# Performance work log

Hardware: AMD Instinct MI355X
Metric: run time of the kernel (lower is better)

Reference implementation:

```python
import jax, jax.numpy as jnp
import numpy as np

BN_EPS = 1e-5

def _bn(x, gamma, beta):
    # BatchNorm1d in training mode: batch mean / biased variance over nodes
    m = x.mean(axis=0)
    v = x.var(axis=0)
    return gamma * (x - m) * jax.lax.rsqrt(v + BN_EPS) + beta

def setup_inputs() -> dict:
    key = jax.random.key(0)
    ks = jax.random.split(key, 16)
    N, E, G = 50000, 600000, 1000
    A, H, O, L = 64, 128, 256, 3
    x = jax.random.normal(ks[0], (N, A), dtype=jnp.float32)
    edge_index = jax.random.randint(ks[1], (2, E), 0, N, dtype=jnp.int64)
    batch_index = jnp.sort(jax.random.randint(ks[2], (N,), 0, G, dtype=jnp.int64))
    s = 1.0 / np.sqrt(H)
    params = {
        "emb_W": jax.random.normal(ks[3], (A, H), jnp.float32) / np.sqrt(A),
        "emb_b": jnp.zeros((H,), jnp.float32),
        "W1": jax.random.normal(ks[4], (L, H, H), jnp.float32) * s,
        "b1": jnp.zeros((L, H), jnp.float32),
        "g1": jnp.ones((L, H), jnp.float32),
        "be1": jnp.zeros((L, H), jnp.float32),
        "W2": jax.random.normal(ks[5], (L, H, H), jnp.float32) * s,
        "b2": jnp.zeros((L, H), jnp.float32),
        "g2": jnp.ones((L, H), jnp.float32),
        "be2": jnp.zeros((L, H), jnp.float32),
        "eps": jnp.zeros((L,), jnp.float32),
        "proj_W": jax.random.normal(ks[6], (H, O), jnp.float32) * s,
        "proj_b": jnp.zeros((O,), jnp.float32),
    }
    return dict(x=x, edge_index=edge_index, batch_index=batch_index, num_graphs=G, **params)

def reference(x, edge_index, batch_index, num_graphs, emb_W, emb_b,
              W1, b1, g1, be1, W2, b2, g2, be2, eps, proj_W, proj_b):
    N = x.shape[0]
    row, col = edge_index[0], edge_index[1]
    h = x @ emb_W + emb_b  # [N, H]
    L = W1.shape[0]
    for l in range(L):
        # gather neighbor feats + scatter-add aggregation
        agg = jax.ops.segment_sum(h[col], row, num_segments=N)
        z = (1.0 + eps[l]) * h + agg
        z = jax.nn.relu(_bn(z @ W1[l] + b1[l], g1[l], be1[l]))
        h = jax.nn.relu(_bn(z @ W2[l] + b2[l], g2[l], be2[l]))
    # graph readout: scatter-add nodes into per-graph sums
    pooled = jax.ops.segment_sum(h, batch_index, num_segments=num_graphs)  # [G, H]
    return pooled @ proj_W + proj_b  # [G, O]
```

## Files before the change

### kernel.cpp

```cpp
#include <hip/hip_runtime.h>
#include <stdint.h>

#define NN 50000
#define NE 600000
#define NG 1000
#define AD 64
#define HD 128
#define OD 256
#define BN_EPS_F 1e-5f
#define INV_N (1.0f / 50000.0f)
#define NB 196
#define FILLB 586
#define PREWB 416
#define NCOPY 32
#define SREG (NCOPY * 256)

typedef __attribute__((ext_vector_type(8))) short  mbf16x8;
typedef __attribute__((ext_vector_type(4))) float  mf32x4;
typedef __attribute__((ext_vector_type(4))) unsigned short mu16x4;
typedef __attribute__((ext_vector_type(4))) unsigned int   mu32x4;

__device__ __forceinline__ float bf2f(unsigned short u) {
    union { unsigned int i; float f; } v; v.i = ((unsigned int)u) << 16; return v.f;
}
__device__ __forceinline__ unsigned short f2bf(float f) {
    union { float f; unsigned int i; } v; v.f = f;
    unsigned int r = v.i + 0x7fffu + ((v.i >> 16) & 1u);
    return (unsigned short)(r >> 16);
}
__device__ __forceinline__ void bn_ss(
    const float* stats, const float* __restrict__ gamma,
    const float* __restrict__ beta, int c, float& sc, float& sh)
{
    const float mean = stats[c] * INV_N;
    const float var = fmaxf(stats[128 + c] * INV_N - mean * mean, 0.f);
    const float inv = rsqrtf(var + BN_EPS_F);
    sc = gamma[c] * inv;
    sh = beta[c] - mean * sc;
}
__device__ __forceinline__ float fold_stat(const float* __restrict__ reg, int t)
{
    float a = 0.f;
#pragma unroll
    for (int c = 0; c < NCOPY; c++) a += reg[c * 256 + t];
    return a;
}

__global__ __launch_bounds__(256) void prew_kernel(
    const float* __restrict__ emb_W, const float* __restrict__ W1,
    const float* __restrict__ W2, unsigned short* __restrict__ wt,
    float* __restrict__ stats, const int* __restrict__ ei,
    int* __restrict__ deg)
{
    if ((int)blockIdx.x >= PREWB) {
        const int e0 = ((blockIdx.x - PREWB) * 256 + threadIdx.x) * 4;
        if (e0 < NE) {
            const int4 rv = *(const int4*)(ei + e0);
            if ((unsigned)rv.x < NN) atomicAdd(&deg[rv.x], 1);
            if ((unsigned)rv.y < NN) atomicAdd(&deg[rv.y], 1);
            if ((unsigned)rv.z < NN) atomicAdd(&deg[rv.z], 1);
            if ((unsigned)rv.w < NN) atomicAdd(&deg[rv.w], 1);
        }
        return;
    }
    const int t = blockIdx.x * 256 + threadIdx.x;
    if (t < 6 * SREG) stats[t] = 0.f;
    if (t < 8192) {
        wt[t] = f2bf(emb_W[(t & 63) * 128 + (t >> 6)]);
    } else {
        const int t2 = t - 8192;
        if (t2 >= 6 * 16384) return;
        const int which = t2 >> 14, o = t2 & 16383;
        const int n = o >> 7, k = o & 127;
        const float* src = (which < 3) ? (W1 + (size_t)which * 16384)
                                       : (W2 + (size_t)(which - 3) * 16384);
        wt[t] = f2bf(src[k * 128 + n]);
    }
}

template <int K, int RG, int AMODE, bool SOUT, int TAIL>
__global__ __launch_bounds__(256) void gemm_kernel(
    const void* __restrict__ in, const unsigned short* __restrict__ Wt,
    const float* __restrict__ bias, const float* __restrict__ stats_in,
    const float* __restrict__ gamma, const float* __restrict__ beta,
    unsigned short* __restrict__ out, float* __restrict__ stats_out, int n_rows,
    const int* __restrict__ t_a, int* __restrict__ t_b, int* __restrict__ t_c)
{
    constexpr int TAILB = (TAIL == 1) ? FILLB : (TAIL == 2) ? NB : 0;
    if (TAIL != 0 && (int)blockIdx.x < TAILB) {
        const int t = blockIdx.x * 256 + threadIdx.x;
        if constexpr (TAIL == 1) {
            const int e0 = t * 4;
            if (e0 < NE) {
                const int4 rv = *(const int4*)(t_a + e0);
                const int4 cv = *(const int4*)(t_a + NE + e0);
                if ((unsigned)rv.x < NN && (unsigned)cv.x < NN)
                    t_c[atomicAdd(&t_b[rv.x], 1)] = cv.x;
                if ((unsigned)rv.y < NN && (unsigned)cv.y < NN)
                    t_c[atomicAdd(&t_b[rv.y], 1)] = cv.y;
                if ((unsigned)rv.z < NN && (unsigned)cv.z < NN)
                    t_c[atomicAdd(&t_b[rv.z], 1)] = cv.z;
                if ((unsigned)rv.w < NN && (unsigned)cv.w < NN)
                    t_c[atomicAdd(&t_b[rv.w], 1)] = cv.w;
            }
        } else {
            if (t < NN) {
                int b = t_a[t];
                int pb = (t == 0) ? -1 : t_a[t - 1];
                if (b > NG - 1) b = NG - 1;
                if (pb > NG - 1) pb = NG - 1;
                for (int g = pb + 1; g <= b; g++) t_b[g] = t;
                if (t == NN - 1)
                    for (int g = b + 1; g <= NG; g++) t_b[g] = NN;
            }
        }
        return;
    }
    const int bid = blockIdx.x - TAILB;

    constexpr int ROWS = RG * 64;
    constexpr int SA = K + 8;
    __shared__ unsigned short zs[ROWS * SA];
    __shared__ float ssl[128], ssh[128];
    __shared__ float lsum[128], lsq[128];
    __shared__ float sarr[256];

    const int tid = threadIdx.x;
    const int wave = tid >> 6, lane = tid & 63;
    const int row0 = bid * ROWS;

    if (SOUT && tid < 128) { lsum[tid] = 0.f; lsq[tid] = 0.f; }
    if (AMODE == 2) {
        sarr[tid] = fold_stat(stats_in, tid);
        __syncthreads();
        if (tid < 128) {
            float sc, sh; bn_ss(sarr, gamma, beta, tid, sc, sh);
            ssl[tid] = sc; ssh[tid] = sh;
        }
        __syncthreads();
    }

    if constexpr (AMODE == 0) {
        const float* src = (const float*)in;
        constexpr int LPR = K / 4;
        for (int i = tid; i < ROWS * LPR; i += 256) {
            const int r = i / LPR, c4 = (i % LPR) * 4;
            mf32x4 v = {0.f, 0.f, 0.f, 0.f};
            if (row0 + r < n_rows)
                v = *(const mf32x4*)(src + (size_t)(row0 + r) * K + c4);
            mu16x4 o;
            o[0] = f2bf(v[0]); o[1] = f2bf(v[1]); o[2] = f2bf(v[2]); o[3] = f2bf(v[3]);
            *(mu16x4*)(&zs[r * SA + c4]) = o;
        }
    } else {
        const unsigned short* src = (const unsigned short*)in;
        constexpr int LPR = K / 8;
        float sc[8], sh[8];
        if constexpr (AMODE == 2) {
            const int c8 = (tid % LPR) * 8;
#pragma unroll
            for (int j = 0; j < 8; j++) { sc[j] = ssl[c8 + j]; sh[j] = ssh[c8 + j]; }
        }
        for (int i = tid; i < ROWS * LPR; i += 256) {
            const int r = i / LPR, c8 = (i % LPR) * 8;
            mu32x4 v = {0, 0, 0, 0};
            if (row0 + r < n_rows)
                v = *(const mu32x4*)(src + (size_t)(row0 + r) * K + c8);
            if constexpr (AMODE == 2) {
                const unsigned short* u = (const unsigned short*)&v;
                mu16x4 oa, ob;
#pragma unroll
                for (int j = 0; j < 4; j++)
                    oa[j] = f2bf(fmaxf(bf2f(u[j]) * sc[j] + sh[j], 0.f));
#pragma unroll
                for (int j = 0; j < 4; j++)
                    ob[j] = f2bf(fmaxf(bf2f(u[4 + j]) * sc[4 + j] + sh[4 + j], 0.f));
                *(mu16x4*)(&zs[r * SA + c8]) = oa;
                *(mu16x4*)(&zs[r * SA + c8 + 4]) = ob;
            } else {
                *(mu32x4*)(&zs[r * SA + c8]) = v;
            }
        }
    }
    __syncthreads();

    mf32x4 acc[RG][8];
#pragma unroll
    for (int g = 0; g < RG; g++)
#pragma unroll
        for (int t = 0; t < 8; t++) acc[g][t] = {0.f, 0.f, 0.f, 0.f};
    const int kq = (lane >> 4) * 8;
    int mrow[RG];
#pragma unroll
    for (int g = 0; g < RG; g++) mrow[g] = wave * (16 * RG) + g * 16 + (lane & 15);
    const unsigned short* wn = Wt + (lane & 15) * K;
#pragma unroll 1
    for (int kk = 0; kk < K / 32; kk++) {
        const int k0 = kk * 32 + kq;
        mbf16x8 a[RG];
#pragma unroll
        for (int g = 0; g < RG; g++) a[g] = *(const mbf16x8*)(&zs[mrow[g] * SA + k0]);
        mbf16x8 bfr[8];
#pragma unroll
        for (int t = 0; t < 8; t++) bfr[t] = *(const mbf16x8*)(wn + t * 16 * K + k0);
#pragma unroll
        for (int t = 0; t < 8; t++)
#pragma unroll
            for (int g = 0; g < RG; g++)
                acc[g][t] = __builtin_amdgcn_mfma_f32_16x16x32_bf16(
                    a[g], bfr[t], acc[g][t], 0, 0, 0);
    }

#pragma unroll
    for (int g = 0; g < RG; g++) {
        const int rbase = wave * (16 * RG) + g * 16 + ((lane >> 4) << 2);
#pragma unroll
        for (int t = 0; t < 8; t++) {
            const int c = t * 16 + (lane & 15);
            const float bv = bias[c];
            float s = 0.f, q = 0.f;
#pragma unroll
            for (int r = 0; r < 4; r++) {
                const int grow = row0 + rbase + r;
                const float y = acc[g][t][r] + bv;
                if (grow < n_rows) {
                    out[(size_t)grow * 128 + c] = f2bf(y);
                    if (SOUT) { s += y; q += y * y; }
                }
            }
            if (SOUT) {
                s += __shfl_xor(s, 16); s += __shfl_xor(s, 32);
                q += __shfl_xor(q, 16); q += __shfl_xor(q, 32);
                if ((lane >> 4) == 0) {
                    atomicAdd(&lsum[c], s);
                    atomicAdd(&lsq[c], q);
                }
            }
        }
    }
    if (SOUT) {
        __syncthreads();
        float* cb = stats_out + (bid & (NCOPY - 1)) * 256;
        if (tid < 128) {
            atomicAdd(&cb[tid], lsum[tid]);
            atomicAdd(&cb[128 + tid], lsq[tid]);
        }
    }
}

__global__ __launch_bounds__(256) void bscan_kernel(
    const int* __restrict__ deg, int* __restrict__ rowptr, int* __restrict__ bsum)
{
    __shared__ int sm[256];
    const int t = threadIdx.x, idx = blockIdx.x * 256 + t;
    const int d = (idx < NN) ? deg[idx] : 0;
    sm[t] = d; __syncthreads();
    for (int ofs = 1; ofs < 256; ofs <<= 1) {
        int v = (t >= ofs) ? sm[t - ofs] : 0;
        __syncthreads();
        sm[t] += v;
        __syncthreads();
    }
    if (idx < NN) rowptr[idx] = sm[t] - d;
    if (t == 255) bsum[blockIdx.x] = sm[255];
}

__global__ __launch_bounds__(256) void scanfix_kernel(
    const int* __restrict__ bsum, int* __restrict__ rowptr, int* __restrict__ cursor)
{
    __shared__ int sm[256];
    const int t = threadIdx.x;
    const int d = (t < NB) ? bsum[t] : 0;
    sm[t] = d; __syncthreads();
    for (int ofs = 1; ofs < 256; ofs <<= 1) {
        int v = (t >= ofs) ? sm[t - ofs] : 0;
        __syncthreads();
        sm[t] += v;
        __syncthreads();
    }
    const int boff = (blockIdx.x == 0) ? 0 : sm[blockIdx.x - 1];
    const int idx = blockIdx.x * 256 + t;
    if (idx < NN) {
        const int v = rowptr[idx] + boff;
        rowptr[idx] = v;
        cursor[idx] = v;
    }
    if (blockIdx.x == NB - 1 && t == 0) rowptr[NN] = sm[NB - 1];
}

template <bool BN>
__global__ __launch_bounds__(256) void gather_kernel(
    const unsigned short* __restrict__ src, const int* __restrict__ rowptr,
    const int* __restrict__ adj, const float* __restrict__ stats,
    const float* __restrict__ gamma, const float* __restrict__ beta,
    const float* __restrict__ eps, int l, unsigned short* __restrict__ z)
{
    __shared__ float sarr[256];
    if constexpr (BN) {
        sarr[threadIdx.x] = fold_stat(stats, threadIdx.x);
        __syncthreads();
    }
    const int node = blockIdx.x * 16 + (threadIdx.x >> 4);
    const int c0 = (threadIdx.x & 15) * 8;
    if (node >= NN) return;
    float sc[8], sh[8];
    if (BN) {
#pragma unroll
        for (int j = 0; j < 8; j++) bn_ss(sarr, gamma, beta, c0 + j, sc[j], sh[j]);
    }
    const float e = 1.0f + eps[l];
    float acc[8];
    {
        mu32x4 v = *(const mu32x4*)(src + (size_t)node * HD + c0);
        const unsigned short* u = (const unsigned short*)&v;
#pragma unroll
        for (int j = 0; j < 8; j++) {
            float f = bf2f(u[j]);
            if (BN) f = fmaxf(f * sc[j] + sh[j], 0.f);
            acc[j] = e * f;
        }
    }
    const int s = rowptr[node], t = rowptr[node + 1];
    int i = s;
    for (; i + 4 <= t; i += 4) {
        const int n0 = adj[i], n1 = adj[i + 1], n2 = adj[i + 2], n3 = adj[i + 3];
        mu32x4 v0 = *(const mu32x4*)(src + (size_t)n0 * HD + c0);
        mu32x4 v1 = *(const mu32x4*)(src + (size_t)n1 * HD + c0);
        mu32x4 v2 = *(const mu32x4*)(src + (size_t)n2 * HD + c0);
        mu32x4 v3 = *(const mu32x4*)(src + (size_t)n3 * HD + c0);
        const unsigned short* u0 = (const unsigned short*)&v0;
        const unsigned short* u1 = (const unsigned short*)&v1;
        const unsigned short* u2 = (const unsigned short*)&v2;
        const unsigned short* u3 = (const unsigned short*)&v3;
#pragma unroll
        for (int j = 0; j < 8; j++) {
            float f0 = bf2f(u0[j]), f1 = bf2f(u1[j]);
            float f2 = bf2f(u2[j]), f3 = bf2f(u3[j]);
            if (BN) {
                f0 = fmaxf(f0 * sc[j] + sh[j], 0.f);
                f1 = fmaxf(f1 * sc[j] + sh[j], 0.f);
                f2 = fmaxf(f2 * sc[j] + sh[j], 0.f);
                f3 = fmaxf(f3 * sc[j] + sh[j], 0.f);
            }
            acc[j] += (f0 + f1) + (f2 + f3);
        }
    }
    for (; i < t; i++) {
        mu32x4 v = *(const mu32x4*)(src + (size_t)adj[i] * HD + c0);
        const unsigned short* u = (const unsigned short*)&v;
#pragma unroll
        for (int j = 0; j < 8; j++) {
            float f = bf2f(u[j]);
            if (BN) f = fmaxf(f * sc[j] + sh[j], 0.f);
            acc[j] += f;
        }
    }
    mu16x4 o0, o1;
#pragma unroll
    for (int j = 0; j < 4; j++) o0[j] = f2bf(acc[j]);
#pragma unroll
    for (int j = 0; j < 4; j++) o1[j] = f2bf(acc[4 + j]);
    *(mu16x4*)(z + (size_t)node * HD + c0) = o0;
    *(mu16x4*)(z + (size_t)node * HD + c0 + 4) = o1;
}

__global__ __launch_bounds__(256) void poolfinal_kernel(
    const unsigned short* __restrict__ y, const int* __restrict__ start,
    const float* __restrict__ stats, const float* __restrict__ gamma,
    const float* __restrict__ beta, const float* __restrict__ pw,
    const float* __restrict__ pb, float* __restrict__ out)
{
    __shared__ float red[16][128];
    __shared__ float pl[128];
    __shared__ float sarr[256];
    sarr[threadIdx.x] = fold_stat(stats, threadIdx.x);
    __syncthreads();
    const int g = blockIdx.x;
    const int rg = threadIdx.x >> 4;
    const int c0 = (threadIdx.x & 15) * 8;
    float sc[8], sh[8];
#pragma unroll
    for (int j = 0; j < 8; j++) bn_ss(sarr, gamma, beta, c0 + j, sc[j], sh[j]);
    int s = start[g], e = start[g + 1];
    if (s < 0) s = 0;
    if (e > NN) e = NN;
    float acc[8];
#pragma unroll
    for (int j = 0; j < 8; j++) acc[j] = 0.f;
    for (int n = s + rg; n < e; n += 16) {
        mu32x4 v = *(const mu32x4*)(y + (size_t)n * HD + c0);
        const unsigned short* u = (const unsigned short*)&v;
#pragma unroll
        for (int j = 0; j < 8; j++)
            acc[j] += fmaxf(bf2f(u[j]) * sc[j] + sh[j], 0.f);
    }
#pragma unroll
    for (int j = 0; j < 8; j++) red[rg][c0 + j] = acc[j];
    __syncthreads();
    if (threadIdx.x < 128) {
        float a = 0.f;
#pragma unroll
        for (int k = 0; k < 16; k++) a += red[k][threadIdx.x];
        pl[threadIdx.x] = a;
    }
    __syncthreads();
    const int o = threadIdx.x;
    float facc = pb[o];
#pragma unroll 4
    for (int k = 0; k < 128; k++) facc += pl[k] * pw[k * 256 + o];
    out[(size_t)g * 256 + o] = facc;
}

extern "C" void kernel_launch(void* const* d_in, const int* in_sizes, int n_in,
                              void* d_out, int out_size, void* d_ws, size_t ws_size,
                              hipStream_t stream)
{
    const float* x      = (const float*)d_in[0];
    const int*   edge   = (const int*)d_in[1];
    const int*   batch  = (const int*)d_in[2];
    const float* emb_W  = (const float*)d_in[4];
    const float* emb_b  = (const float*)d_in[5];
    const float* W1     = (const float*)d_in[6];
    const float* b1     = (const float*)d_in[7];
    const float* g1     = (const float*)d_in[8];
    const float* be1    = (const float*)d_in[9];
    const float* W2     = (const float*)d_in[10];
    const float* b2     = (const float*)d_in[11];
    const float* g2     = (const float*)d_in[12];
    const float* be2    = (const float*)d_in[13];
    const float* eps    = (const float*)d_in[14];
    const float* proj_W = (const float*)d_in[15];
    const float* proj_b = (const float*)d_in[16];
    float* out = (float*)d_out;

    char* ws = (char*)d_ws;
    size_t off = 0;
    auto take = [&](size_t bytes) -> char* {
        char* p = ws + off;
        off += (bytes + 255) & ~(size_t)255;
        return p;
    };
    float*          stats  = (float*)take(6 * SREG * 4);
    int*            start  = (int*)take((NG + 1) * 4);
    int*            deg    = (int*)take(NN * 4);
    int*            rowptr = (int*)take((NN + 1) * 4);
    int*            cursor = (int*)take(NN * 4);
    int*            bsum   = (int*)take(256 * 4);
    unsigned short* wt     = (unsigned short*)take((size_t)(8192 + 6 * 16384) * 2);
    int*            adj    = (int*)take((size_t)NE * 4);
    unsigned short* zbuf   = (unsigned short*)take((size_t)NN * HD * 2);
    unsigned short* y1buf  = (unsigned short*)take((size_t)NN * HD * 2);
    unsigned short* y2buf  = (unsigned short*)take((size_t)NN * HD * 2);

    const int eg_grid = (NN + 63) / 64;
    const int lg_grid = (NN + 127) / 128;
    auto st = [&](int r) { return stats + (size_t)r * SREG; };

    hipMemsetAsync(deg, 0, NN * 4, stream);
    prew_kernel<<<PREWB + FILLB, 256, 0, stream>>>(
        emb_W, W1, W2, wt, stats, edge, deg);
    bscan_kernel<<<NB, 256, 0, stream>>>(deg, rowptr, bsum);
    scanfix_kernel<<<NB, 256, 0, stream>>>(bsum, rowptr, cursor);

    gemm_kernel<AD, 1, 0, false, 1><<<FILLB + eg_grid, 256, 0, stream>>>(
        x, wt, emb_b, nullptr, nullptr, nullptr, y2buf, nullptr, NN,
        edge, cursor, adj);

    for (int l = 0; l < 3; l++) {
        if (l == 0)
            gather_kernel<false><<<(NN + 15) / 16, 256, 0, stream>>>(
                y2buf, rowptr, adj, nullptr, nullptr, nullptr, eps, l, zbuf);
        else
            gather_kernel<true><<<(NN + 15) / 16, 256, 0, stream>>>(
                y2buf, rowptr, adj, st(2 * l - 1),
                g2 + (l - 1) * HD, be2 + (l - 1) * HD, eps, l, zbuf);
        gemm_kernel<HD, 2, 1, true, 0><<<lg_grid, 256, 0, stream>>>(
            zbuf, wt + 8192 + (size_t)l * 16384, b1 + l * HD,
            nullptr, nullptr, nullptr, y1buf, st(2 * l), NN,
            nullptr, nullptr, nullptr);
        if (l < 2)
            gemm_kernel<HD, 2, 2, true, 0><<<lg_grid, 256, 0, stream>>>(
                y1buf, wt + 8192 + (size_t)(3 + l) * 16384, b2 + l * HD,
                st(2 * l), g1 + l * HD, be1 + l * HD, y2buf, st(2 * l + 1), NN,
                nullptr, nullptr, nullptr);
        else
            gemm_kernel<HD, 2, 2, true, 2><<<NB + lg_grid, 256, 0, stream>>>(
                y1buf, wt + 8192 + (size_t)(3 + l) * 16384, b2 + l * HD,
                st(2 * l), g1 + l * HD, be1 + l * HD, y2buf, st(2 * l + 1), NN,
                batch, start, nullptr);
    }

    poolfinal_kernel<<<NG, 256, 0, stream>>>(
        y2buf, start, st(5), g2 + 2 * HD, be2 + 2 * HD, proj_W, proj_b, out);
}
```

Before: 404.3 us.

## Stage per-block adjacency in LDS and deepen gather unroll; widen embed GEMM tiles

The gather kernel now loads each block's 16 row pointers and up to 768 adjacency indices into shared memory in one cooperative pass. It then issues 8 neighbor row loads at a time instead of 4, giving more memory-level parallelism on the random gathers. The CSR fill tail now handles 8 edges per thread over half as many blocks, and the embedding GEMM uses 2 row groups per block, which halves its grid. The costs are two extra barriers and more register pressure from the wider loads. The early return for out-of-range nodes is gone, but 50000 divides evenly by 16, so nothing reads out of bounds.

```diff
diff --git a/kernel.cpp b/kernel.cpp
--- a/kernel.cpp
+++ b/kernel.cpp
@@ -10,10 +10,12 @@
 #define BN_EPS_F 1e-5f
 #define INV_N (1.0f / 50000.0f)
 #define NB 196
-#define FILLB 586
+#define FILLB 293
+#define DEGB 586
 #define PREWB 416
 #define NCOPY 32
 #define SREG (NCOPY * 256)
+#define SADJ 768
 
 typedef __attribute__((ext_vector_type(8))) short  mbf16x8;
 typedef __attribute__((ext_vector_type(4))) float  mf32x4;
@@ -90,18 +92,28 @@
     if (TAIL != 0 && (int)blockIdx.x < TAILB) {
         const int t = blockIdx.x * 256 + threadIdx.x;
         if constexpr (TAIL == 1) {
-            const int e0 = t * 4;
+            const int e0 = t * 8;
             if (e0 < NE) {
-                const int4 rv = *(const int4*)(t_a + e0);
-                const int4 cv = *(const int4*)(t_a + NE + e0);
-                if ((unsigned)rv.x < NN && (unsigned)cv.x < NN)
-                    t_c[atomicAdd(&t_b[rv.x], 1)] = cv.x;
-                if ((unsigned)rv.y < NN && (unsigned)cv.y < NN)
-                    t_c[atomicAdd(&t_b[rv.y], 1)] = cv.y;
-                if ((unsigned)rv.z < NN && (unsigned)cv.z < NN)
-                    t_c[atomicAdd(&t_b[rv.z], 1)] = cv.z;
-                if ((unsigned)rv.w < NN && (unsigned)cv.w < NN)
-                    t_c[atomicAdd(&t_b[rv.w], 1)] = cv.w;
+                const int4 r0 = *(const int4*)(t_a + e0);
+                const int4 r1 = *(const int4*)(t_a + e0 + 4);
+                const int4 c0 = *(const int4*)(t_a + NE + e0);
+                const int4 c1 = *(const int4*)(t_a + NE + e0 + 4);
+                if ((unsigned)r0.x < NN && (unsigned)c0.x < NN)
+                    t_c[atomicAdd(&t_b[r0.x], 1)] = c0.x;
+                if ((unsigned)r0.y < NN && (unsigned)c0.y < NN)
+                    t_c[atomicAdd(&t_b[r0.y], 1)] = c0.y;
+                if ((unsigned)r0.z < NN && (unsigned)c0.z < NN)
+                    t_c[atomicAdd(&t_b[r0.z], 1)] = c0.z;
+                if ((unsigned)r0.w < NN && (unsigned)c0.w < NN)
+                    t_c[atomicAdd(&t_b[r0.w], 1)] = c0.w;
+                if ((unsigned)r1.x < NN && (unsigned)c1.x < NN)
+                    t_c[atomicAdd(&t_b[r1.x], 1)] = c1.x;
+                if ((unsigned)r1.y < NN && (unsigned)c1.y < NN)
+                    t_c[atomicAdd(&t_b[r1.y], 1)] = c1.y;
+                if ((unsigned)r1.z < NN && (unsigned)c1.z < NN)
+                    t_c[atomicAdd(&t_b[r1.z], 1)] = c1.z;
+                if ((unsigned)r1.w < NN && (unsigned)c1.w < NN)
+                    t_c[atomicAdd(&t_b[r1.w], 1)] = c1.w;
             }
         } else {
             if (t < NN) {
@@ -296,19 +308,26 @@
     const float* __restrict__ eps, int l, unsigned short* __restrict__ z)
 {
     __shared__ float sarr[256];
-    if constexpr (BN) {
-        sarr[threadIdx.x] = fold_stat(stats, threadIdx.x);
-        __syncthreads();
-    }
-    const int node = blockIdx.x * 16 + (threadIdx.x >> 4);
-    const int c0 = (threadIdx.x & 15) * 8;
-    if (node >= NN) return;
+    __shared__ int srp[17];
+    __shared__ int sadj[SADJ];
+    const int tid = threadIdx.x;
+    if constexpr (BN) sarr[tid] = fold_stat(stats, tid);
+    const int n0 = blockIdx.x * 16;
+    if (tid < 17) srp[tid] = rowptr[n0 + tid];
+    __syncthreads();
+    const int base = srp[0];
+    const int total = srp[16] - base;
+    for (int i = tid; i < total && i < SADJ; i += 256) sadj[i] = adj[base + i];
+    __syncthreads();
+
+    const int node = n0 + (tid >> 4);
+    const int c0 = (tid & 15) * 8;
     float sc[8], sh[8];
     if (BN) {
 #pragma unroll
         for (int j = 0; j < 8; j++) bn_ss(sarr, gamma, beta, c0 + j, sc[j], sh[j]);
     }
-    const float e = 1.0f + eps[l];
+    const float e1 = 1.0f + eps[l];
     float acc[8];
     {
         mu32x4 v = *(const mu32x4*)(src + (size_t)node * HD + c0);
@@ -317,36 +336,50 @@
         for (int j = 0; j < 8; j++) {
             float f = bf2f(u[j]);
             if (BN) f = fmaxf(f * sc[j] + sh[j], 0.f);
-            acc[j] = e * f;
-        }
-    }
-    const int s = rowptr[node], t = rowptr[node + 1];
+            acc[j] = e1 * f;
+        }
+    }
+    const int s = srp[tid >> 4] - base;
+    const int e = srp[(tid >> 4) + 1] - base;
+    auto nb_at = [&](int i) -> int {
+        return (i < SADJ) ? sadj[i] : adj[base + i];
+    };
     int i = s;
-    for (; i + 4 <= t; i += 4) {
-        const int n0 = adj[i], n1 = adj[i + 1], n2 = adj[i + 2], n3 = adj[i + 3];
-        mu32x4 v0 = *(const mu32x4*)(src + (size_t)n0 * HD + c0);
-        mu32x4 v1 = *(const mu32x4*)(src + (size_t)n1 * HD + c0);
-        mu32x4 v2 = *(const mu32x4*)(src + (size_t)n2 * HD + c0);
-        mu32x4 v3 = *(const mu32x4*)(src + (size_t)n3 * HD + c0);
-        const unsigned short* u0 = (const unsigned short*)&v0;
-        const unsigned short* u1 = (const unsigned short*)&v1;
-        const unsigned short* u2 = (const unsigned short*)&v2;
-        const unsigned short* u3 = (const unsigned short*)&v3;
-#pragma unroll
-        for (int j = 0; j < 8; j++) {
-            float f0 = bf2f(u0[j]), f1 = bf2f(u1[j]);
-            float f2 = bf2f(u2[j]), f3 = bf2f(u3[j]);
-            if (BN) {
-                f0 = fmaxf(f0 * sc[j] + sh[j], 0.f);
-                f1 = fmaxf(f1 * sc[j] + sh[j], 0.f);
-                f2 = fmaxf(f2 * sc[j] + sh[j], 0.f);
-                f3 = fmaxf(f3 * sc[j] + sh[j], 0.f);
-            }
-            acc[j] += (f0 + f1) + (f2 + f3);
-        }
-    }
-    for (; i < t; i++) {
-        mu32x4 v = *(const mu32x4*)(src + (size_t)adj[i] * HD + c0);
+    for (; i + 8 <= e; i += 8) {
+        mu32x4 v[8];
+#pragma unroll
+        for (int k = 0; k < 8; k++)
+            v[k] = *(const mu32x4*)(src + (size_t)nb_at(i + k) * HD + c0);
+#pragma unroll
+        for (int k = 0; k < 8; k++) {
+            const unsigned short* u = (const unsigned short*)&v[k];
+#pragma unroll
+            for (int j = 0; j < 8; j++) {
+                float f = bf2f(u[j]);
+                if (BN) f = fmaxf(f * sc[j] + sh[j], 0.f);
+                acc[j] += f;
+            }
+        }
+    }
+    if (i + 4 <= e) {
+        mu32x4 v[4];
+#pragma unroll
+        for (int k = 0; k < 4; k++)
+            v[k] = *(const mu32x4*)(src + (size_t)nb_at(i + k) * HD + c0);
+#pragma unroll
+        for (int k = 0; k < 4; k++) {
+            const unsigned short* u = (const unsigned short*)&v[k];
+#pragma unroll
+            for (int j = 0; j < 8; j++) {
+                float f = bf2f(u[j]);
+                if (BN) f = fmaxf(f * sc[j] + sh[j], 0.f);
+                acc[j] += f;
+            }
+        }
+        i += 4;
+    }
+    for (; i < e; i++) {
+        mu32x4 v = *(const mu32x4*)(src + (size_t)nb_at(i) * HD + c0);
         const unsigned short* u = (const unsigned short*)&v;
 #pragma unroll
         for (int j = 0; j < 8; j++) {
@@ -452,17 +485,17 @@
     unsigned short* y1buf  = (unsigned short*)take((size_t)NN * HD * 2);
     unsigned short* y2buf  = (unsigned short*)take((size_t)NN * HD * 2);
 
-    const int eg_grid = (NN + 63) / 64;
+    const int eg_grid = (NN + 127) / 128;
     const int lg_grid = (NN + 127) / 128;
     auto st = [&](int r) { return stats + (size_t)r * SREG; };
 
     hipMemsetAsync(deg, 0, NN * 4, stream);
-    prew_kernel<<<PREWB + FILLB, 256, 0, stream>>>(
+    prew_kernel<<<PREWB + DEGB, 256, 0, stream>>>(
         emb_W, W1, W2, wt, stats, edge, deg);
     bscan_kernel<<<NB, 256, 0, stream>>>(deg, rowptr, bsum);
     scanfix_kernel<<<NB, 256, 0, stream>>>(bsum, rowptr, cursor);
 
-    gemm_kernel<AD, 1, 0, false, 1><<<FILLB + eg_grid, 256, 0, stream>>>(
+    gemm_kernel<AD, 2, 0, false, 1><<<FILLB + eg_grid, 256, 0, stream>>>(
         x, wt, emb_b, nullptr, nullptr, nullptr, y2buf, nullptr, NN,
         edge, cursor, adj);
 
```

New measurement: 435.2 us. 1.08x slower.
